# Optimization experiments

Measured on AMD Instinct MI355X. Metric: run time of the kernel, lower is better.

## Reference

```python
import jax, jax.numpy as jnp
import numpy as np

K_CLASSES = 5   # num support classes (5-way)
N_SHOT = 5      # supports per class


def setup_inputs() -> dict:
    key = jax.random.key(0)
    k0, k1, k2, k3 = jax.random.split(key, 4)
    b, bs, c, h, w = 32, K_CLASSES * N_SHOT, 512, 14, 14
    dk, dv = 128, 128
    return {
        "support_features": jax.random.normal(k0, (bs, c, h, w), jnp.float32),
        "query_features": jax.random.normal(k1, (b, c, h, w), jnp.float32),
        "support_labels": jnp.repeat(jnp.arange(K_CLASSES), N_SHOT).astype(jnp.int32),
        "W_qk": jax.random.normal(k2, (dk, c), jnp.float32) * 0.02,  # 1x1 conv weight
        "W_v": jax.random.normal(k3, (dv, c), jnp.float32) * 0.02,   # 1x1 conv weight
    }


def reference(support_features, query_features, support_labels, W_qk, W_v):
    scale = 1.0  # 1/temperature, temperature=1.0
    # 1x1 convs == channel-mixing einsums
    query_q = jnp.einsum('bchw,dc->bdhw', query_features, W_qk)
    query_v = jnp.einsum('bchw,dc->bdhw', query_features, W_v)
    supp_k = jnp.einsum('nchw,dc->ndhw', support_features, W_qk)
    supp_v = jnpveinsum = jnp.einsum('nchw,dc->ndhw', support_features, W_v)
    supp_v = jnpveinsum
    b, cv, h, w = query_v.shape

    # similarity over all supports: [b,h,w,n,i,j] (contracts dim_key)
    sim = jnp.einsum('bchw,ncij->bhwnij', query_q, supp_k) * scale

    # per-class masked softmax over the (n,i,j) axes restricted to that class's
    # supports == index_select + softmax in the original loop (labels balanced).
    cls_mask = support_labels[None, :] == jnp.arange(K_CLASSES)[:, None]  # [K,n]
    neg = jnp.finfo(sim.dtype).min
    sim_k = jnp.where(cls_mask[:, None, None, None, :, None, None], sim[None], neg)  # [K,b,h,w,n,i,j]
    attn = jax.nn.softmax(sim_k.reshape(K_CLASSES, b, h, w, -1), axis=-1)
    attn = attn.reshape(sim_k.shape)  # masked-out entries -> exactly 0

    # weighted sum of support values: [K,b,c,h,w]
    out = jnp.einsum('kbhwnij,ncij->kbchw', attn, supp_v)
    prototypes = jnp.transpose(out, (1, 0, 2, 3, 4)).reshape(b, K_CLASSES, -1)  # b k (c h w)
    query_v_flat = query_v.reshape(b, 1, -1)  # b () (c h w)
    return prototypes, query_v_flat
```

## Files before the change

### kernel.cpp

```cpp
#include <hip/hip_runtime.h>
#include <cstdint>
#include <cstddef>

#define NB   32
#define NSUP 25
#define KCLS 5
#define NC   512
#define ND   128
#define NP   196
#define JS   208
#define SHIFT 8.0f

#define KPITCH 272
#define KTILE  (16 * KPITCH)
#define KBUF   (2 * KTILE)
#define VPITCH 80
#define VBUF   (128 * VPITCH)
#define BUFSZ  (KBUF + VBUF)

#define NGRP   (NB * KCLS * 13)
#define PACC_F ((size_t)NGRP * 2 * 2048)
#define PSUM_F ((size_t)NGRP * 2 * 16)

typedef __attribute__((ext_vector_type(8))) short short8;
typedef __attribute__((ext_vector_type(4))) float floatx4;

__device__ inline short f2bf(float x) {
  union { float f; uint32_t u; } v; v.f = x;
  uint32_t r = (v.u + 0x7FFFu + ((v.u >> 16) & 1u)) >> 16;
  return (short)(r & 0xFFFFu);
}
__device__ inline uint32_t pk2(float a, float b) {
  return (uint32_t)(uint16_t)f2bf(a) | ((uint32_t)(uint16_t)f2bf(b) << 16);
}

__global__ __launch_bounds__(256) void wconv_kernel(
    const float* __restrict__ Wqk, const float* __restrict__ Wv,
    uint16_t* __restrict__ Whi)
{
  const int f = (blockIdx.x * 256 + (int)threadIdx.x) * 8;
  const float* src = (f < ND * NC) ? (Wqk + f) : (Wv + f - ND * NC);
  short8 hv;
  #pragma unroll
  for (int i = 0; i < 8; ++i) hv[i] = f2bf(src[i]);
  *(short8*)(Whi + f) = hv;
}

__global__ __launch_bounds__(256) void gemm_kernel(
    const float* __restrict__ supp, const float* __restrict__ qry,
    const uint16_t* __restrict__ Whi,
    uint16_t* __restrict__ Qt, uint16_t* __restrict__ Kt,
    uint16_t* __restrict__ Vt, float* __restrict__ outVq)
{
  __shared__ uint16_t xs[16 * 520];
  const int bx = blockIdx.x;
  const int t16 = bx % 13, img = bx / 13;
  const int tid = (int)threadIdx.x;
  const int w = tid >> 6, lane = tid & 63, ln = lane & 15, q = lane >> 4;
  const int d0 = w * 32;
  const int p0 = t16 * 16;

  const float* __restrict__ X = (img < NB)
      ? (qry  + (size_t)img * NC * NP)
      : (supp + (size_t)(img - NB) * NC * NP);

  #pragma unroll
  for (int k = 0; k < 4; ++k) {
    const int id = k * 256 + tid;
    const int cp = id >> 2;
    const int pq = id & 3;
    int pg = p0 + pq * 4; if (pg > NP - 4) pg = NP - 4;
    const floatx4 fa = *(const floatx4*)(X + (2 * cp) * NP + pg);
    const floatx4 fb = *(const floatx4*)(X + (2 * cp + 1) * NP + pg);
    #pragma unroll
    for (int i = 0; i < 4; ++i)
      *((uint32_t*)xs + (pq * 4 + i) * 260 + cp) = pk2(fa[i], fb[i]);
  }
  __syncthreads();

  floatx4 aQ[2], aV[2];
  #pragma unroll
  for (int nt = 0; nt < 2; ++nt) {
    aQ[nt] = (floatx4){0.f, 0.f, 0.f, 0.f};
    aV[nt] = (floatx4){0.f, 0.f, 0.f, 0.f};
  }

  for (int ks = 0; ks < 16; ++ks) {
    const short8 xh = *(const short8*)&xs[ln * 520 + ks * 32 + q * 8];
    #pragma unroll
    for (int nt = 0; nt < 2; ++nt) {
      const size_t wr = (size_t)(d0 + nt * 16 + ln) * NC + ks * 32 + q * 8;
      const short8 wqh = *(const short8*)(Whi + wr);
      aQ[nt] = __builtin_amdgcn_mfma_f32_16x16x32_bf16(xh, wqh, aQ[nt], 0, 0, 0);
      const short8 wvh = *(const short8*)(Whi + (size_t)ND * NC + wr);
      aV[nt] = __builtin_amdgcn_mfma_f32_16x16x32_bf16(wvh, xh, aV[nt], 0, 0, 0);
    }
  }

  if (img < NB) {
    #pragma unroll
    for (int nt = 0; nt < 2; ++nt)
      #pragma unroll
      for (int rr = 0; rr < 4; ++rr) {
        const int p = p0 + q * 4 + rr;
        if (p < NP)
          Qt[((size_t)img * NP + p) * ND + d0 + nt * 16 + ln] = (uint16_t)f2bf(aQ[nt][rr]);
      }
  } else {
    const int n = img - NB;
    #pragma unroll
    for (int nt = 0; nt < 2; ++nt)
      #pragma unroll
      for (int rr = 0; rr < 4; ++rr) {
        const int p = p0 + q * 4 + rr;
        Kt[((size_t)n * JS + p) * ND + d0 + nt * 16 + ln] = (uint16_t)f2bf(aQ[nt][rr]);
      }
  }
  const int p = p0 + ln;
  if (img < NB) {
    if (p < NP) {
      #pragma unroll
      for (int nt = 0; nt < 2; ++nt)
        #pragma unroll
        for (int rr = 0; rr < 4; ++rr)
          outVq[((size_t)img * ND + d0 + nt * 16 + q * 4 + rr) * NP + p] = aV[nt][rr];
    }
  } else {
    const int n = img - NB;
    #pragma unroll
    for (int nt = 0; nt < 2; ++nt)
      #pragma unroll
      for (int rr = 0; rr < 4; ++rr)
        Vt[((size_t)n * ND + d0 + nt * 16 + q * 4 + rr) * JS + p] = (uint16_t)f2bf(aV[nt][rr]);
  }
}

template <int NCHUNK, bool PART>
__global__ __launch_bounds__(256, 2) void attn_kernel(
    const uint16_t* __restrict__ Qt, const uint16_t* __restrict__ Kt,
    const uint16_t* __restrict__ Vt, const int* __restrict__ labels,
    float* __restrict__ out, float* __restrict__ pacc, float* __restrict__ psum)
{
  __shared__ __align__(16) char smem[2 * BUFSZ];

  const int bx = blockIdx.x;
  const int pt = bx % 13;
  const int rem = bx / 13;
  const int kc = rem % KCLS;
  const int rest = rem / KCLS;
  const int oct = PART ? (rest & 3) : rest;
  const int half = PART ? (rest >> 2) : 0;
  const int c0 = half * NCHUNK;
  const int b0 = oct * 8;
  const int p0 = pt * 16;
  const int tid = (int)threadIdx.x;
  const int w = tid >> 6, lane = tid & 63, ln = lane & 15, q = lane >> 4;
  const int bA = b0 + w * 2, bB = bA + 1;

  const int myl = (lane < NSUP) ? labels[lane] : -1;
  unsigned long long m = __ballot(myl == kc);
  int clsPack = 0;
  #pragma unroll
  for (int s = 0; s < 5; ++s) {
    const int n = (m != 0ull) ? (int)__builtin_ctzll(m) : 0;
    clsPack |= n << (6 * s);
    m &= (m - 1);
  }

  short8 aqA[4], aqB[4];
  {
    int p = p0 + ln; if (p > NP - 1) p = NP - 1;
    const uint16_t* baseA = Qt + ((size_t)bA * NP + p) * ND + q * 8;
    const uint16_t* baseB = Qt + ((size_t)bB * NP + p) * ND + q * 8;
    #pragma unroll
    for (int ks = 0; ks < 4; ++ks) {
      aqA[ks] = *(const short8*)(baseA + ks * 32);
      aqB[ks] = *(const short8*)(baseB + ks * 32);
    }
  }

  floatx4 accA[8], accB[8];
  #pragma unroll
  for (int dt = 0; dt < 8; ++dt) {
    accA[dt] = (floatx4){0.f, 0.f, 0.f, 0.f};
    accB[dt] = (floatx4){0.f, 0.f, 0.f, 0.f};
  }
  float SsA = 0.f, SsB = 0.f;

  const int alo = (ln + ((q & 1) << 5)) << 2;
  const bool hiTile = (q >= 2);

  int4 pf[4];
  {
    int nk[2], j0k[2], nv[2], jv[2];
    #pragma unroll
    for (int t = 0; t < 2; ++t) {
      const int tile16 = c0 * 2 + t;
      int s = tile16 / 13;
      j0k[t] = (tile16 - s * 13) * 16;
      if (s > 4) s = 4;
      nk[t] = (clsPack >> (6 * s)) & 63;
    }
    #pragma unroll
    for (int h = 0; h < 2; ++h) {
      const int ch = c0 * 32 + h * 16;
      int sv = ch / JS, jvv = ch - sv * JS;
      if (sv > 4) { sv = 4; jvv = 192; }
      nv[h] = (clsPack >> (6 * sv)) & 63;
      jv[h] = jvv;
    }
    #pragma unroll
    for (int pass = 0; pass < 4; ++pass) {
      const int slot = pass * 256 + tid;
      if (pass < 2) {
        const int t = slot >> 8, r = (slot >> 4) & 15, sc = slot & 15;
        pf[pass] = *(const int4*)(Kt + ((size_t)(nk[t] * JS + j0k[t] + r)) * ND + sc * 8);
      } else {
        const int vs = slot - 512;
        const int h = vs >> 8, d = (vs >> 1) & 127, sc2 = vs & 1;
        pf[pass] = *(const int4*)(Vt + ((size_t)(nv[h] * ND + d)) * JS + jv[h] + sc2 * 8);
      }
    }
    char* db = smem;
    #pragma unroll
    for (int pass = 0; pass < 4; ++pass) {
      const int slot = pass * 256 + tid;
      if (pass < 2) {
        const int t = slot >> 8, r = (slot >> 4) & 15, sc = slot & 15;
        *(int4*)(db + t * KTILE + r * KPITCH + sc * 16) = pf[pass];
      } else {
        const int vs = slot - 512;
        const int h = vs >> 8, d = (vs >> 1) & 127, sc2 = vs & 1;
        *(int4*)(db + KBUF + d * VPITCH + (h * 2 + sc2) * 16) = pf[pass];
      }
    }
  }
  __syncthreads();

  for (int li = 0; li < NCHUNK; ++li) {
    const int cc = c0 + li;
    const int nc = cc + 1;
    int nk[2], j0k[2], nv[2], jv[2];
    if (li < NCHUNK - 1) {
      #pragma unroll
      for (int t = 0; t < 2; ++t) {
        const int tile16 = nc * 2 + t;
        int s = tile16 / 13;
        j0k[t] = (tile16 - s * 13) * 16;
        if (s > 4) s = 4;
        nk[t] = (clsPack >> (6 * s)) & 63;
      }
      #pragma unroll
      for (int h = 0; h < 2; ++h) {
        const int ch = nc * 32 + h * 16;
        int sv = ch / JS, jvv = ch - sv * JS;
        if (sv > 4) { sv = 4; jvv = 192; }
        nv[h] = (clsPack >> (6 * sv)) & 63;
        jv[h] = jvv;
      }
      #pragma unroll
      for (int pass = 0; pass < 4; ++pass) {
        const int slot = pass * 256 + tid;
        if (pass < 2) {
          const int t = slot >> 8, r = (slot >> 4) & 15, sc = slot & 15;
          pf[pass] = *(const int4*)(Kt + ((size_t)(nk[t] * JS + j0k[t] + r)) * ND + sc * 8);
        } else {
          const int vs = slot - 512;
          const int h = vs >> 8, d = (vs >> 1) & 127, sc2 = vs & 1;
          pf[pass] = *(const int4*)(Vt + ((size_t)(nv[h] * ND + d)) * JS + jv[h] + sc2 * 8);
        }
      }
    }

    const char* kb = smem + (li & 1) * BUFSZ;
    const char* vb = kb + KBUF;

    short8 av[8];
    #pragma unroll
    for (int dt = 0; dt < 8; ++dt)
      av[dt] = *(const short8*)(vb + (dt * 16 + ln) * VPITCH + q * 16);

    short8 bk[2][4];
    #pragma unroll
    for (int t = 0; t < 2; ++t)
      #pragma unroll
      for (int ks = 0; ks < 4; ++ks)
        bk[t][ks] = *(const short8*)(kb + t * KTILE + ln * KPITCH + ks * 64 + q * 16);

    floatx4 e0A, e1A, e0B, e1B;
    #pragma unroll
    for (int t = 0; t < 2; ++t) {
      const int tile16 = cc * 2 + t;
      const int s = tile16 / 13;
      const int j0 = (tile16 - s * 13) * 16;
      const bool tval = (s < 5);
      floatx4 d4A = {0.f, 0.f, 0.f, 0.f};
      floatx4 d4B = {0.f, 0.f, 0.f, 0.f};
      #pragma unroll
      for (int ks = 0; ks < 4; ++ks) {
        d4A = __builtin_amdgcn_mfma_f32_16x16x32_bf16(bk[t][ks], aqA[ks], d4A, 0, 0, 0);
        d4B = __builtin_amdgcn_mfma_f32_16x16x32_bf16(bk[t][ks], aqB[ks], d4B, 0, 0, 0);
      }
      floatx4 evA, evB;
      #pragma unroll
      for (int r = 0; r < 4; ++r) {
        const int j = j0 + q * 4 + r;
        const bool val = (tval && j < NP);
        const float eA = val ? __expf(d4A[r] - SHIFT) : 0.f;
        const float eB = val ? __expf(d4B[r] - SHIFT) : 0.f;
        evA[r] = eA; SsA += eA;
        evB[r] = eB; SsB += eB;
      }
      if (t == 0) { e0A = evA; e0B = evB; } else { e1A = evA; e1B = evB; }
    }

    short8 bpA, bpB;
    #pragma unroll
    for (int r = 0; r < 4; ++r) {
      const uint32_t peA = pk2(e0A[r], e1A[r]);
      const int loA = __builtin_amdgcn_ds_bpermute(alo, (int)peA);
      const int hiA = __builtin_amdgcn_ds_bpermute(alo + 64, (int)peA);
      bpA[r]     = (short)(uint16_t)(hiTile ? (loA >> 16) : (loA & 0xFFFF));
      bpA[4 + r] = (short)(uint16_t)(hiTile ? (hiA >> 16) : (hiA & 0xFFFF));
      const uint32_t peB = pk2(e0B[r], e1B[r]);
      const int loB = __builtin_amdgcn_ds_bpermute(alo, (int)peB);
      const int hiB = __builtin_amdgcn_ds_bpermute(alo + 64, (int)peB);
      bpB[r]     = (short)(uint16_t)(hiTile ? (loB >> 16) : (loB & 0xFFFF));
      bpB[4 + r] = (short)(uint16_t)(hiTile ? (hiB >> 16) : (hiB & 0xFFFF));
    }

    #pragma unroll
    for (int dt = 0; dt < 8; ++dt) {
      accA[dt] = __builtin_amdgcn_mfma_f32_16x16x32_bf16(av[dt], bpA, accA[dt], 0, 0, 0);
      accB[dt] = __builtin_amdgcn_mfma_f32_16x16x32_bf16(av[dt], bpB, accB[dt], 0, 0, 0);
    }

    if (li < NCHUNK - 1) {
      char* db = smem + ((li + 1) & 1) * BUFSZ;
      #pragma unroll
      for (int pass = 0; pass < 4; ++pass) {
        const int slot = pass * 256 + tid;
        if (pass < 2) {
          const int t = slot >> 8, r = (slot >> 4) & 15, sc = slot & 15;
          *(int4*)(db + t * KTILE + r * KPITCH + sc * 16) = pf[pass];
        } else {
          const int vs = slot - 512;
          const int h = vs >> 8, d = (vs >> 1) & 127, sc2 = vs & 1;
          *(int4*)(db + KBUF + d * VPITCH + (h * 2 + sc2) * 16) = pf[pass];
        }
      }
    }
    __syncthreads();
  }

  float svA = SsA;
  svA += __shfl_xor(svA, 16);
  svA += __shfl_xor(svA, 32);
  float svB = SsB;
  svB += __shfl_xor(svB, 16);
  svB += __shfl_xor(svB, 32);

  if (PART) {
    const size_t grpA = (((size_t)(bA * KCLS + kc)) * 13 + pt) * 2 + half;
    const size_t grpB = (((size_t)(bB * KCLS + kc)) * 13 + pt) * 2 + half;
    float* paA = pacc + grpA * 2048;
    float* paB = pacc + grpB * 2048;
    #pragma unroll
    for (int dt = 0; dt < 8; ++dt)
      #pragma unroll
      for (int rr = 0; rr < 4; ++rr) {
        paA[(dt * 16 + q * 4 + rr) * 16 + ln] = accA[dt][rr];
        paB[(dt * 16 + q * 4 + rr) * 16 + ln] = accB[dt][rr];
      }
    if (q == 0) {
      psum[grpA * 16 + ln] = svA;
      psum[grpB * 16 + ln] = svB;
    }
  } else {
    const int pp = p0 + ln;
    if (pp < NP) {
      const float invA = 1.f / svA, invB = 1.f / svB;
      float* obA = out + ((size_t)(bA * KCLS + kc) * ND + q * 4) * NP + pp;
      float* obB = out + ((size_t)(bB * KCLS + kc) * ND + q * 4) * NP + pp;
      #pragma unroll
      for (int dt = 0; dt < 8; ++dt)
        #pragma unroll
        for (int rr = 0; rr < 4; ++rr) {
          obA[(size_t)(dt * 16 + rr) * NP] = accA[dt][rr] * invA;
          obB[(size_t)(dt * 16 + rr) * NP] = accB[dt][rr] * invB;
        }
    }
  }
}

__global__ __launch_bounds__(256) void merge_kernel(
    const float* __restrict__ pacc, const float* __restrict__ psum,
    float* __restrict__ out)
{
  const int bx = blockIdx.x;
  const int pt = bx % 13;
  const int rem = bx / 13;
  const int tid = (int)threadIdx.x;
  const int ln = tid & 15, dr = tid >> 4;
  const size_t g0 = (((size_t)rem) * 13 + pt) * 2;

  const float s = psum[g0 * 16 + ln] + psum[(g0 + 1) * 16 + ln];
  const int pp = pt * 16 + ln;
  if (pp >= NP) return;
  const float inv = 1.f / s;

  const float* pa0 = pacc + g0 * 2048;
  const float* pa1 = pacc + (g0 + 1) * 2048;
  float* ob = out + (size_t)rem * ND * NP + pp;
  #pragma unroll
  for (int i = 0; i < 8; ++i) {
    const int d = dr * 8 + i;
    ob[(size_t)d * NP] = (pa0[d * 16 + ln] + pa1[d * 16 + ln]) * inv;
  }
}

extern "C" void kernel_launch(void* const* d_in, const int* in_sizes, int n_in,
                              void* d_out, int out_size, void* d_ws, size_t ws_size,
                              hipStream_t stream) {
  const float* supp   = (const float*)d_in[0];
  const float* qry    = (const float*)d_in[1];
  const int*   labels = (const int*)d_in[2];
  const float* Wqk    = (const float*)d_in[3];
  const float* Wv     = (const float*)d_in[4];
  float* out = (float*)d_out;

  uint16_t* Whi = (uint16_t*)d_ws;
  uint16_t* Qt  = Whi + (size_t)2 * ND * NC;
  uint16_t* Kt  = Qt  + (size_t)NB * NP * ND;
  uint16_t* Vt  = Kt  + (size_t)NSUP * JS * ND;
  float* pacc   = (float*)(Vt + (size_t)NSUP * ND * JS);
  float* psum   = pacc + PACC_F;
  const size_t need = (size_t)((char*)(psum + PSUM_F) - (char*)d_ws);
  float* outVq = out + (size_t)NB * KCLS * ND * NP;

  wconv_kernel<<<64, 256, 0, stream>>>(Wqk, Wv, Whi);
  gemm_kernel<<<741, 256, 0, stream>>>(supp, qry, Whi, Qt, Kt, Vt, outVq);
  if (ws_size >= need) {
    attn_kernel<17, true><<<520, 256, 0, stream>>>(Qt, Kt, Vt, labels, out, pacc, psum);
    merge_kernel<<<2080, 256, 0, stream>>>(pacc, psum, out);
  } else {
    attn_kernel<34, false><<<260, 256, 0, stream>>>(Qt, Kt, Vt, labels, out, nullptr, nullptr);
  }
}
```

Before: 164.9 us.

## Stage K/V tiles via direct global-to-LDS loads with XOR-swizzled layout

Replaces the register-staged prefetch of K and V tiles (global load into registers, then a later LDS store) with global_load_lds direct copies into a swizzled, unpadded double buffer. This removes the register pressure and the extra LDS-store pass. Tile index decoding now uses incremental counters instead of divisions. It also swaps software bf16 rounding for the hardware v_cvt_pk_bf16_f32 instruction and adds s_setprio around the MFMA blocks. The risks are in correctness: the swizzle must match the fragment reads, and the V tile addressing at the segment tail changes from clamping to using raw offsets.

After: 169.5 us. 2.8% more time.

```diff
diff --git a/kernel.cpp b/kernel.cpp
--- a/kernel.cpp
+++ b/kernel.cpp
@@ -11,12 +11,8 @@
 #define JS   208
 #define SHIFT 8.0f
 
-#define KPITCH 272
-#define KTILE  (16 * KPITCH)
-#define KBUF   (2 * KTILE)
-#define VPITCH 80
-#define VBUF   (128 * VPITCH)
-#define BUFSZ  (KBUF + VBUF)
+#define ABUF   16384
+#define VOFF   8192
 
 #define NGRP   (NB * KCLS * 13)
 #define PACC_F ((size_t)NGRP * 2 * 2048)
@@ -30,8 +26,15 @@
   uint32_t r = (v.u + 0x7FFFu + ((v.u >> 16) & 1u)) >> 16;
   return (short)(r & 0xFFFFu);
 }
-__device__ inline uint32_t pk2(float a, float b) {
-  return (uint32_t)(uint16_t)f2bf(a) | ((uint32_t)(uint16_t)f2bf(b) << 16);
+__device__ inline uint32_t cvtpk(float lo, float hi) {
+  uint32_t r;
+  asm("v_cvt_pk_bf16_f32 %0, %1, %2" : "=v"(r) : "v"(lo), "v"(hi));
+  return r;
+}
+__device__ __forceinline__ void gl_lds16(const uint16_t* g, char* l) {
+  __builtin_amdgcn_global_load_lds(
+      (const __attribute__((address_space(1))) uint32_t*)g,
+      (__attribute__((address_space(3))) uint32_t*)l, 16, 0, 0);
 }
 
 __global__ __launch_bounds__(256) void wconv_kernel(
@@ -74,7 +77,7 @@
     const floatx4 fb = *(const floatx4*)(X + (2 * cp + 1) * NP + pg);
     #pragma unroll
     for (int i = 0; i < 4; ++i)
-      *((uint32_t*)xs + (pq * 4 + i) * 260 + cp) = pk2(fa[i], fb[i]);
+      *((uint32_t*)xs + (pq * 4 + i) * 260 + cp) = cvtpk(fa[i], fb[i]);
   }
   __syncthreads();
 
@@ -135,13 +138,42 @@
   }
 }
 
+
+#define DECODE2() do {                                                         \
+    _Pragma("unroll")                                                          \
+    for (int t_ = 0; t_ < 2; ++t_) {                                           \
+      dS[t_] = s_ctr; dJ[t_] = j_ctr;                                          \
+      const int sc_ = s_ctr > 4 ? 4 : s_ctr;                                   \
+      dN[t_] = (clsPack >> (6 * sc_)) & 63;                                    \
+      j_ctr += 16; if (j_ctr >= JS) { j_ctr -= JS; s_ctr += 1; }               \
+    }                                                                          \
+  } while (0)
+
+#define STAGE(DB) do {                                                         \
+    if (w < 2) {                                                               \
+      const int kb_ = (dN[w] * JS + dJ[w]) * ND;                               \
+      _Pragma("unroll")                                                        \
+      for (int i_ = 0; i_ < 4; ++i_)                                           \
+        gl_lds16(Kt + kb_ + dKoff[i_], (DB) + w * 4096 + i_ * 1024);           \
+    } else {                                                                   \
+      const int vA_ = dN[0] * (ND * JS) + dJ[0];                               \
+      const int vB_ = dN[1] * (ND * JS) + dJ[1];                               \
+      const int vs_ = hb ? vB_ : vA_;                                          \
+      const int i2b_ = (w & 1) * 4;                                            \
+      _Pragma("unroll")                                                        \
+      for (int k_ = 0; k_ < 4; ++k_)                                           \
+        gl_lds16(Vt + vs_ + (i2b_ + k_) * (16 * JS) + vrow,                    \
+                 (DB) + VOFF + (i2b_ + k_) * 1024);                            \
+    }                                                                          \
+  } while (0)
+
 template <int NCHUNK, bool PART>
 __global__ __launch_bounds__(256, 2) void attn_kernel(
     const uint16_t* __restrict__ Qt, const uint16_t* __restrict__ Kt,
     const uint16_t* __restrict__ Vt, const int* __restrict__ labels,
     float* __restrict__ out, float* __restrict__ pacc, float* __restrict__ psum)
 {
-  __shared__ __align__(16) char smem[2 * BUFSZ];
+  __shared__ __align__(16) char smem[2 * ABUF];
 
   const int bx = blockIdx.x;
   const int pt = bx % 13;
@@ -166,6 +198,7 @@
     clsPack |= n << (6 * s);
     m &= (m - 1);
   }
+  clsPack = __builtin_amdgcn_readfirstlane(clsPack);
 
   short8 aqA[4], aqB[4];
   {
@@ -190,122 +223,71 @@
   const int alo = (ln + ((q & 1) << 5)) << 2;
   const bool hiTile = (q >= 2);
 
-  int4 pf[4];
-  {
-    int nk[2], j0k[2], nv[2], jv[2];
+  const int rK = lane >> 4, scK = lane & 15;
+  int dKoff[4];
+  #pragma unroll
+  for (int i = 0; i < 4; ++i) {
+    const int r = 4 * i + rK;
+    dKoff[i] = r * ND + ((scK ^ (r & 7)) * 8);
+  }
+  const int dV = lane >> 2, s2 = lane & 3;
+  const int s2p = s2 ^ ((dV >> 1) & 3);
+  const int hb = s2p >> 1;
+  const int vrow = dV * JS + (s2p & 1) * 8;
+
+  int kfr[4];
+  #pragma unroll
+  for (int ks = 0; ks < 4; ++ks)
+    kfr[ks] = ln * 256 + (((ks * 4 + q) ^ (ln & 7)) << 4);
+  const int avb = VOFF + ln * 64 + ((q ^ ((ln >> 1) & 3)) << 4);
+
+  int s_ctr = (c0 * 2) / 13;
+  int j_ctr = (c0 * 2 - s_ctr * 13) * 16;
+  int dS[2], dJ[2], dN[2], cS[2], cJ[2];
+
+  DECODE2();
+  STAGE(smem);
+  __syncthreads();
+
+  for (int it = 0; it < NCHUNK; ++it) {
+    #pragma unroll
+    for (int i = 0; i < 2; ++i) { cS[i] = dS[i]; cJ[i] = dJ[i]; }
+    if (it < NCHUNK - 1) {
+      DECODE2();
+      STAGE(smem + ((it + 1) & 1) * ABUF);
+    }
+
+    const char* cb = smem + (it & 1) * ABUF;
+
+    short8 av[8];
+    #pragma unroll
+    for (int dt = 0; dt < 8; ++dt)
+      av[dt] = *(const short8*)(cb + avb + dt * 1024);
+
+    short8 bk[2][4];
+    #pragma unroll
+    for (int t = 0; t < 2; ++t)
+      #pragma unroll
+      for (int ks = 0; ks < 4; ++ks)
+        bk[t][ks] = *(const short8*)(cb + kfr[ks] + t * 4096);
+
+    floatx4 e0A, e1A, e0B, e1B;
     #pragma unroll
     for (int t = 0; t < 2; ++t) {
-      const int tile16 = c0 * 2 + t;
-      int s = tile16 / 13;
-      j0k[t] = (tile16 - s * 13) * 16;
-      if (s > 4) s = 4;
-      nk[t] = (clsPack >> (6 * s)) & 63;
-    }
-    #pragma unroll
-    for (int h = 0; h < 2; ++h) {
-      const int ch = c0 * 32 + h * 16;
-      int sv = ch / JS, jvv = ch - sv * JS;
-      if (sv > 4) { sv = 4; jvv = 192; }
-      nv[h] = (clsPack >> (6 * sv)) & 63;
-      jv[h] = jvv;
-    }
-    #pragma unroll
-    for (int pass = 0; pass < 4; ++pass) {
-      const int slot = pass * 256 + tid;
-      if (pass < 2) {
-        const int t = slot >> 8, r = (slot >> 4) & 15, sc = slot & 15;
-        pf[pass] = *(const int4*)(Kt + ((size_t)(nk[t] * JS + j0k[t] + r)) * ND + sc * 8);
-      } else {
-        const int vs = slot - 512;
-        const int h = vs >> 8, d = (vs >> 1) & 127, sc2 = vs & 1;
-        pf[pass] = *(const int4*)(Vt + ((size_t)(nv[h] * ND + d)) * JS + jv[h] + sc2 * 8);
-      }
-    }
-    char* db = smem;
-    #pragma unroll
-    for (int pass = 0; pass < 4; ++pass) {
-      const int slot = pass * 256 + tid;
-      if (pass < 2) {
-        const int t = slot >> 8, r = (slot >> 4) & 15, sc = slot & 15;
-        *(int4*)(db + t * KTILE + r * KPITCH + sc * 16) = pf[pass];
-      } else {
-        const int vs = slot - 512;
-        const int h = vs >> 8, d = (vs >> 1) & 127, sc2 = vs & 1;
-        *(int4*)(db + KBUF + d * VPITCH + (h * 2 + sc2) * 16) = pf[pass];
-      }
-    }
-  }
-  __syncthreads();
-
-  for (int li = 0; li < NCHUNK; ++li) {
-    const int cc = c0 + li;
-    const int nc = cc + 1;
-    int nk[2], j0k[2], nv[2], jv[2];
-    if (li < NCHUNK - 1) {
-      #pragma unroll
-      for (int t = 0; t < 2; ++t) {
-        const int tile16 = nc * 2 + t;
-        int s = tile16 / 13;
-        j0k[t] = (tile16 - s * 13) * 16;
-        if (s > 4) s = 4;
-        nk[t] = (clsPack >> (6 * s)) & 63;
-      }
-      #pragma unroll
-      for (int h = 0; h < 2; ++h) {
-        const int ch = nc * 32 + h * 16;
-        int sv = ch / JS, jvv = ch - sv * JS;
-        if (sv > 4) { sv = 4; jvv = 192; }
-        nv[h] = (clsPack >> (6 * sv)) & 63;
-        jv[h] = jvv;
-      }
-      #pragma unroll
-      for (int pass = 0; pass < 4; ++pass) {
-        const int slot = pass * 256 + tid;
-        if (pass < 2) {
-          const int t = slot >> 8, r = (slot >> 4) & 15, sc = slot & 15;
-          pf[pass] = *(const int4*)(Kt + ((size_t)(nk[t] * JS + j0k[t] + r)) * ND + sc * 8);
-        } else {
-          const int vs = slot - 512;
-          const int h = vs >> 8, d = (vs >> 1) & 127, sc2 = vs & 1;
-          pf[pass] = *(const int4*)(Vt + ((size_t)(nv[h] * ND + d)) * JS + jv[h] + sc2 * 8);
-        }
-      }
-    }
-
-    const char* kb = smem + (li & 1) * BUFSZ;
-    const char* vb = kb + KBUF;
-
-    short8 av[8];
-    #pragma unroll
-    for (int dt = 0; dt < 8; ++dt)
-      av[dt] = *(const short8*)(vb + (dt * 16 + ln) * VPITCH + q * 16);
-
-    short8 bk[2][4];
-    #pragma unroll
-    for (int t = 0; t < 2; ++t)
-      #pragma unroll
-      for (int ks = 0; ks < 4; ++ks)
-        bk[t][ks] = *(const short8*)(kb + t * KTILE + ln * KPITCH + ks * 64 + q * 16);
-
-    floatx4 e0A, e1A, e0B, e1B;
-    #pragma unroll
-    for (int t = 0; t < 2; ++t) {
-      const int tile16 = cc * 2 + t;
-      const int s = tile16 / 13;
-      const int j0 = (tile16 - s * 13) * 16;
-      const bool tval = (s < 5);
       floatx4 d4A = {0.f, 0.f, 0.f, 0.f};
       floatx4 d4B = {0.f, 0.f, 0.f, 0.f};
+      __builtin_amdgcn_s_setprio(1);
       #pragma unroll
       for (int ks = 0; ks < 4; ++ks) {
         d4A = __builtin_amdgcn_mfma_f32_16x16x32_bf16(bk[t][ks], aqA[ks], d4A, 0, 0, 0);
         d4B = __builtin_amdgcn_mfma_f32_16x16x32_bf16(bk[t][ks], aqB[ks], d4B, 0, 0, 0);
       }
+      __builtin_amdgcn_s_setprio(0);
       floatx4 evA, evB;
       #pragma unroll
       for (int r = 0; r < 4; ++r) {
-        const int j = j0 + q * 4 + r;
-        const bool val = (tval && j < NP);
+        const int j = cJ[t] + q * 4 + r;
+        const bool val = (cS[t] < 5 && j < NP);
         const float eA = val ? __expf(d4A[r] - SHIFT) : 0.f;
         const float eB = val ? __expf(d4B[r] - SHIFT) : 0.f;
         evA[r] = eA; SsA += eA;
@@ -317,39 +299,26 @@
     short8 bpA, bpB;
     #pragma unroll
     for (int r = 0; r < 4; ++r) {
-      const uint32_t peA = pk2(e0A[r], e1A[r]);
+      const uint32_t peA = cvtpk(e0A[r], e1A[r]);
       const int loA = __builtin_amdgcn_ds_bpermute(alo, (int)peA);
       const int hiA = __builtin_amdgcn_ds_bpermute(alo + 64, (int)peA);
       bpA[r]     = (short)(uint16_t)(hiTile ? (loA >> 16) : (loA & 0xFFFF));
       bpA[4 + r] = (short)(uint16_t)(hiTile ? (hiA >> 16) : (hiA & 0xFFFF));
-      const uint32_t peB = pk2(e0B[r], e1B[r]);
+      const uint32_t peB = cvtpk(e0B[r], e1B[r]);
       const int loB = __builtin_amdgcn_ds_bpermute(alo, (int)peB);
       const int hiB = __builtin_amdgcn_ds_bpermute(alo + 64, (int)peB);
       bpB[r]     = (short)(uint16_t)(hiTile ? (loB >> 16) : (loB & 0xFFFF));
       bpB[4 + r] = (short)(uint16_t)(hiTile ? (hiB >> 16) : (hiB & 0xFFFF));
     }
 
+    __builtin_amdgcn_s_setprio(1);
     #pragma unroll
     for (int dt = 0; dt < 8; ++dt) {
       accA[dt] = __builtin_amdgcn_mfma_f32_16x16x32_bf16(av[dt], bpA, accA[dt], 0, 0, 0);
       accB[dt] = __builtin_amdgcn_mfma_f32_16x16x32_bf16(av[dt], bpB, accB[dt], 0, 0, 0);
     }
-
-    if (li < NCHUNK - 1) {
-      char* db = smem + ((li + 1) & 1) * BUFSZ;
-      #pragma unroll
-      for (int pass = 0; pass < 4; ++pass) {
-        const int slot = pass * 256 + tid;
-        if (pass < 2) {
-          const int t = slot >> 8, r = (slot >> 4) & 15, sc = slot & 15;
-          *(int4*)(db + t * KTILE + r * KPITCH + sc * 16) = pf[pass];
-        } else {
-          const int vs = slot - 512;
-          const int h = vs >> 8, d = (vs >> 1) & 127, sc2 = vs & 1;
-          *(int4*)(db + KBUF + d * VPITCH + (h * 2 + sc2) * 16) = pf[pass];
-        }
-      }
-    }
+    __builtin_amdgcn_s_setprio(0);
+
     __syncthreads();
   }
 
```

## Load V fragments directly from global into registers and use hardware bf16 pack

Applied to the files above, without the earlier changes.

Stops staging the V tile through shared memory. Each lane now loads its MFMA A-operand fragments for V straight from global memory at the start of each chunk, and the shared buffer holds only the double-buffered K tiles. This removes the LDS writes and reads for V and shrinks LDS use, which can help occupancy. In exchange, V loads are issued in the same iteration they are used, so they are no longer prefetched a chunk ahead and their latency may be exposed. The software float-to-bf16 rounding is also replaced with the v_cvt_pk_bf16_f32 instruction.

Measured after the change: 175.2 us. 1.06x slower.

```diff
diff --git a/kernel.cpp b/kernel.cpp
--- a/kernel.cpp
+++ b/kernel.cpp
@@ -14,9 +14,6 @@
 #define KPITCH 272
 #define KTILE  (16 * KPITCH)
 #define KBUF   (2 * KTILE)
-#define VPITCH 80
-#define VBUF   (128 * VPITCH)
-#define BUFSZ  (KBUF + VBUF)
 
 #define NGRP   (NB * KCLS * 13)
 #define PACC_F ((size_t)NGRP * 2 * 2048)
@@ -30,8 +27,10 @@
   uint32_t r = (v.u + 0x7FFFu + ((v.u >> 16) & 1u)) >> 16;
   return (short)(r & 0xFFFFu);
 }
-__device__ inline uint32_t pk2(float a, float b) {
-  return (uint32_t)(uint16_t)f2bf(a) | ((uint32_t)(uint16_t)f2bf(b) << 16);
+__device__ inline uint32_t cvtpk(float lo, float hi) {
+  uint32_t r;
+  asm("v_cvt_pk_bf16_f32 %0, %1, %2" : "=v"(r) : "v"(lo), "v"(hi));
+  return r;
 }
 
 __global__ __launch_bounds__(256) void wconv_kernel(
@@ -74,7 +73,7 @@
     const floatx4 fb = *(const floatx4*)(X + (2 * cp + 1) * NP + pg);
     #pragma unroll
     for (int i = 0; i < 4; ++i)
-      *((uint32_t*)xs + (pq * 4 + i) * 260 + cp) = pk2(fa[i], fb[i]);
+      *((uint32_t*)xs + (pq * 4 + i) * 260 + cp) = cvtpk(fa[i], fb[i]);
   }
   __syncthreads();
 
@@ -141,7 +140,7 @@
     const uint16_t* __restrict__ Vt, const int* __restrict__ labels,
     float* __restrict__ out, float* __restrict__ pacc, float* __restrict__ psum)
 {
-  __shared__ __align__(16) char smem[2 * BUFSZ];
+  __shared__ __align__(16) char smem[2 * KBUF];
 
   const int bx = blockIdx.x;
   const int pt = bx % 13;
@@ -190,9 +189,10 @@
   const int alo = (ln + ((q & 1) << 5)) << 2;
   const bool hiTile = (q >= 2);
 
-  int4 pf[4];
+  int4 pf[2];
+  int cnv[2], cjv[2];
   {
-    int nk[2], j0k[2], nv[2], jv[2];
+    int nk[2], j0k[2];
     #pragma unroll
     for (int t = 0; t < 2; ++t) {
       const int tile16 = c0 * 2 + t;
@@ -206,33 +206,20 @@
       const int ch = c0 * 32 + h * 16;
       int sv = ch / JS, jvv = ch - sv * JS;
       if (sv > 4) { sv = 4; jvv = 192; }
-      nv[h] = (clsPack >> (6 * sv)) & 63;
-      jv[h] = jvv;
-    }
-    #pragma unroll
-    for (int pass = 0; pass < 4; ++pass) {
+      cnv[h] = (clsPack >> (6 * sv)) & 63;
+      cjv[h] = jvv;
+    }
+    #pragma unroll
+    for (int pass = 0; pass < 2; ++pass) {
       const int slot = pass * 256 + tid;
-      if (pass < 2) {
-        const int t = slot >> 8, r = (slot >> 4) & 15, sc = slot & 15;
-        pf[pass] = *(const int4*)(Kt + ((size_t)(nk[t] * JS + j0k[t] + r)) * ND + sc * 8);
-      } else {
-        const int vs = slot - 512;
-        const int h = vs >> 8, d = (vs >> 1) & 127, sc2 = vs & 1;
-        pf[pass] = *(const int4*)(Vt + ((size_t)(nv[h] * ND + d)) * JS + jv[h] + sc2 * 8);
-      }
-    }
-    char* db = smem;
-    #pragma unroll
-    for (int pass = 0; pass < 4; ++pass) {
+      const int t = slot >> 8, r = (slot >> 4) & 15, sc = slot & 15;
+      pf[pass] = *(const int4*)(Kt + ((size_t)(nk[t] * JS + j0k[t] + r)) * ND + sc * 8);
+    }
+    #pragma unroll
+    for (int pass = 0; pass < 2; ++pass) {
       const int slot = pass * 256 + tid;
-      if (pass < 2) {
-        const int t = slot >> 8, r = (slot >> 4) & 15, sc = slot & 15;
-        *(int4*)(db + t * KTILE + r * KPITCH + sc * 16) = pf[pass];
-      } else {
-        const int vs = slot - 512;
-        const int h = vs >> 8, d = (vs >> 1) & 127, sc2 = vs & 1;
-        *(int4*)(db + KBUF + d * VPITCH + (h * 2 + sc2) * 16) = pf[pass];
-      }
+      const int t = slot >> 8, r = (slot >> 4) & 15, sc = slot & 15;
+      *(int4*)(smem + t * KTILE + r * KPITCH + sc * 16) = pf[pass];
     }
   }
   __syncthreads();
@@ -240,8 +227,19 @@
   for (int li = 0; li < NCHUNK; ++li) {
     const int cc = c0 + li;
     const int nc = cc + 1;
-    int nk[2], j0k[2], nv[2], jv[2];
+
+    const int nvh = hiTile ? cnv[1] : cnv[0];
+    const int jvh = hiTile ? cjv[1] : cjv[0];
+    const uint16_t* vr = Vt + ((size_t)nvh * ND + ln) * JS + jvh + (q & 1) * 8;
+    short8 av[8];
+    #pragma unroll
+    for (int dt = 0; dt < 8; ++dt)
+      av[dt] = *(const short8*)(vr + (size_t)(dt * 16) * JS);
+    __builtin_amdgcn_sched_barrier(0);
+
+    int nnv[2], njv[2];
     if (li < NCHUNK - 1) {
+      int nk[2], j0k[2];
       #pragma unroll
       for (int t = 0; t < 2; ++t) {
         const int tile16 = nc * 2 + t;
@@ -255,30 +253,18 @@
         const int ch = nc * 32 + h * 16;
         int sv = ch / JS, jvv = ch - sv * JS;
         if (sv > 4) { sv = 4; jvv = 192; }
-        nv[h] = (clsPack >> (6 * sv)) & 63;
-        jv[h] = jvv;
-      }
-      #pragma unroll
-      for (int pass = 0; pass < 4; ++pass) {
+        nnv[h] = (clsPack >> (6 * sv)) & 63;
+        njv[h] = jvv;
+      }
+      #pragma unroll
+      for (int pass = 0; pass < 2; ++pass) {
         const int slot = pass * 256 + tid;
-        if (pass < 2) {
-          const int t = slot >> 8, r = (slot >> 4) & 15, sc = slot & 15;
-          pf[pass] = *(const int4*)(Kt + ((size_t)(nk[t] * JS + j0k[t] + r)) * ND + sc * 8);
-        } else {
-          const int vs = slot - 512;
-          const int h = vs >> 8, d = (vs >> 1) & 127, sc2 = vs & 1;
-          pf[pass] = *(const int4*)(Vt + ((size_t)(nv[h] * ND + d)) * JS + jv[h] + sc2 * 8);
-        }
-      }
-    }
-
-    const char* kb = smem + (li & 1) * BUFSZ;
-    const char* vb = kb + KBUF;
-
-    short8 av[8];
-    #pragma unroll
-    for (int dt = 0; dt < 8; ++dt)
-      av[dt] = *(const short8*)(vb + (dt * 16 + ln) * VPITCH + q * 16);
+        const int t = slot >> 8, r = (slot >> 4) & 15, sc = slot & 15;
+        pf[pass] = *(const int4*)(Kt + ((size_t)(nk[t] * JS + j0k[t] + r)) * ND + sc * 8);
+      }
+    }
+
+    const char* kb = smem + (li & 1) * KBUF;
 
     short8 bk[2][4];
     #pragma unroll
@@ -317,12 +303,12 @@
     short8 bpA, bpB;
     #pragma unroll
     for (int r = 0; r < 4; ++r) {
-      const uint32_t peA = pk2(e0A[r], e1A[r]);
+      const uint32_t peA = cvtpk(e0A[r], e1A[r]);
       const int loA = __builtin_amdgcn_ds_bpermute(alo, (int)peA);
       const int hiA = __builtin_amdgcn_ds_bpermute(alo + 64, (int)peA);
       bpA[r]     = (short)(uint16_t)(hiTile ? (loA >> 16) : (loA & 0xFFFF));
       bpA[4 + r] = (short)(uint16_t)(hiTile ? (hiA >> 16) : (hiA & 0xFFFF));
-      const uint32_t peB = pk2(e0B[r], e1B[r]);
+      const uint32_t peB = cvtpk(e0B[r], e1B[r]);
       const int loB = __builtin_amdgcn_ds_bpermute(alo, (int)peB);
       const int hiB = __builtin_amdgcn_ds_bpermute(alo + 64, (int)peB);
       bpB[r]     = (short)(uint16_t)(hiTile ? (loB >> 16) : (loB & 0xFFFF));
@@ -336,19 +322,15 @@
     }
 
     if (li < NCHUNK - 1) {
-      char* db = smem + ((li + 1) & 1) * BUFSZ;
-      #pragma unroll
-      for (int pass = 0; pass < 4; ++pass) {
+      char* db = smem + ((li + 1) & 1) * KBUF;
+      #pragma unroll
+      for (int pass = 0; pass < 2; ++pass) {
         const int slot = pass * 256 + tid;
-        if (pass < 2) {
-          const int t = slot >> 8, r = (slot >> 4) & 15, sc = slot & 15;
-          *(int4*)(db + t * KTILE + r * KPITCH + sc * 16) = pf[pass];
-        } else {
-          const int vs = slot - 512;
-          const int h = vs >> 8, d = (vs >> 1) & 127, sc2 = vs & 1;
-          *(int4*)(db + KBUF + d * VPITCH + (h * 2 + sc2) * 16) = pf[pass];
-        }
-      }
+        const int t = slot >> 8, r = (slot >> 4) & 15, sc = slot & 15;
+        *(int4*)(db + t * KTILE + r * KPITCH + sc * 16) = pf[pass];
+      }
+      cnv[0] = nnv[0]; cnv[1] = nnv[1];
+      cjv[0] = njv[0]; cjv[1] = njv[1];
     }
     __syncthreads();
   }
```

## Fuse split-K merge into attention via atomic last-block finalize; use hw bf16 pack

Applied to the files above, without the earlier changes.

Removes the separate merge kernel. Each attention block still writes its partial accumulators and sums, then bumps a per-tile atomic counter. The block that arrives second reads its partner's partial, combines it with its own register accumulators, normalizes, and writes the output directly. This saves one launch and half of the partial-buffer reads. It relies on the flag counters starting even and on the atomic-parity protocol staying correct across repeated calls. It also replaces the software bf16 round-and-pack with the v_cvt_pk_bf16_f32 instruction.

Measured after the change: 254.5 us. 1.54x slower.

```diff
diff --git a/kernel.cpp b/kernel.cpp
--- a/kernel.cpp
+++ b/kernel.cpp
@@ -21,6 +21,7 @@
 #define NGRP   (NB * KCLS * 13)
 #define PACC_F ((size_t)NGRP * 2 * 2048)
 #define PSUM_F ((size_t)NGRP * 2 * 16)
+#define NPAIR  (4 * KCLS * 13)
 
 typedef __attribute__((ext_vector_type(8))) short short8;
 typedef __attribute__((ext_vector_type(4))) float floatx4;
@@ -30,8 +31,10 @@
   uint32_t r = (v.u + 0x7FFFu + ((v.u >> 16) & 1u)) >> 16;
   return (short)(r & 0xFFFFu);
 }
-__device__ inline uint32_t pk2(float a, float b) {
-  return (uint32_t)(uint16_t)f2bf(a) | ((uint32_t)(uint16_t)f2bf(b) << 16);
+__device__ inline uint32_t cvtpk(float lo, float hi) {
+  uint32_t r;
+  asm("v_cvt_pk_bf16_f32 %0, %1, %2" : "=v"(r) : "v"(lo), "v"(hi));
+  return r;
 }
 
 __global__ __launch_bounds__(256) void wconv_kernel(
@@ -74,7 +77,7 @@
     const floatx4 fb = *(const floatx4*)(X + (2 * cp + 1) * NP + pg);
     #pragma unroll
     for (int i = 0; i < 4; ++i)
-      *((uint32_t*)xs + (pq * 4 + i) * 260 + cp) = pk2(fa[i], fb[i]);
+      *((uint32_t*)xs + (pq * 4 + i) * 260 + cp) = cvtpk(fa[i], fb[i]);
   }
   __syncthreads();
 
@@ -139,7 +142,8 @@
 __global__ __launch_bounds__(256, 2) void attn_kernel(
     const uint16_t* __restrict__ Qt, const uint16_t* __restrict__ Kt,
     const uint16_t* __restrict__ Vt, const int* __restrict__ labels,
-    float* __restrict__ out, float* __restrict__ pacc, float* __restrict__ psum)
+    float* __restrict__ out, float* __restrict__ pacc, float* __restrict__ psum,
+    int* __restrict__ flags)
 {
   __shared__ __align__(16) char smem[2 * BUFSZ];
 
@@ -317,12 +321,12 @@
     short8 bpA, bpB;
     #pragma unroll
     for (int r = 0; r < 4; ++r) {
-      const uint32_t peA = pk2(e0A[r], e1A[r]);
+      const uint32_t peA = cvtpk(e0A[r], e1A[r]);
       const int loA = __builtin_amdgcn_ds_bpermute(alo, (int)peA);
       const int hiA = __builtin_amdgcn_ds_bpermute(alo + 64, (int)peA);
       bpA[r]     = (short)(uint16_t)(hiTile ? (loA >> 16) : (loA & 0xFFFF));
       bpA[4 + r] = (short)(uint16_t)(hiTile ? (hiA >> 16) : (hiA & 0xFFFF));
-      const uint32_t peB = pk2(e0B[r], e1B[r]);
+      const uint32_t peB = cvtpk(e0B[r], e1B[r]);
       const int loB = __builtin_amdgcn_ds_bpermute(alo, (int)peB);
       const int hiB = __builtin_amdgcn_ds_bpermute(alo + 64, (int)peB);
       bpB[r]     = (short)(uint16_t)(hiTile ? (loB >> 16) : (loB & 0xFFFF));
@@ -361,10 +365,10 @@
   svB += __shfl_xor(svB, 32);
 
   if (PART) {
-    const size_t grpA = (((size_t)(bA * KCLS + kc)) * 13 + pt) * 2 + half;
-    const size_t grpB = (((size_t)(bB * KCLS + kc)) * 13 + pt) * 2 + half;
-    float* paA = pacc + grpA * 2048;
-    float* paB = pacc + grpB * 2048;
+    const size_t gA = (((size_t)(bA * KCLS + kc)) * 13 + pt) * 2 + half;
+    const size_t gB = (((size_t)(bB * KCLS + kc)) * 13 + pt) * 2 + half;
+    float* paA = pacc + gA * 2048;
+    float* paB = pacc + gB * 2048;
     #pragma unroll
     for (int dt = 0; dt < 8; ++dt)
       #pragma unroll
@@ -373,8 +377,38 @@
         paB[(dt * 16 + q * 4 + rr) * 16 + ln] = accB[dt][rr];
       }
     if (q == 0) {
-      psum[grpA * 16 + ln] = svA;
-      psum[grpB * 16 + ln] = svB;
+      psum[gA * 16 + ln] = svA;
+      psum[gB * 16 + ln] = svB;
+    }
+    __threadfence();
+    __syncthreads();
+    if (tid == 0)
+      ((int*)smem)[0] = atomicAdd(&flags[(oct * KCLS + kc) * 13 + pt], 1);
+    __syncthreads();
+    const int old = ((int*)smem)[0];
+    if (old & 1) {
+      __threadfence();
+      const size_t gAo = (((size_t)(bA * KCLS + kc)) * 13 + pt) * 2 + (1 - half);
+      const size_t gBo = (((size_t)(bB * KCLS + kc)) * 13 + pt) * 2 + (1 - half);
+      const float svAt = svA + psum[gAo * 16 + ln];
+      const float svBt = svB + psum[gBo * 16 + ln];
+      const int pp = p0 + ln;
+      if (pp < NP) {
+        const float invA = 1.f / svAt, invB = 1.f / svBt;
+        const float* qaA = pacc + gAo * 2048;
+        const float* qaB = pacc + gBo * 2048;
+        float* obA = out + ((size_t)(bA * KCLS + kc) * ND + q * 4) * NP + pp;
+        float* obB = out + ((size_t)(bB * KCLS + kc) * ND + q * 4) * NP + pp;
+        #pragma unroll
+        for (int dt = 0; dt < 8; ++dt)
+          #pragma unroll
+          for (int rr = 0; rr < 4; ++rr) {
+            obA[(size_t)(dt * 16 + rr) * NP] =
+                (accA[dt][rr] + qaA[(dt * 16 + q * 4 + rr) * 16 + ln]) * invA;
+            obB[(size_t)(dt * 16 + rr) * NP] =
+                (accB[dt][rr] + qaB[(dt * 16 + q * 4 + rr) * 16 + ln]) * invB;
+          }
+      }
     }
   } else {
     const int pp = p0 + ln;
@@ -390,32 +424,6 @@
           obB[(size_t)(dt * 16 + rr) * NP] = accB[dt][rr] * invB;
         }
     }
-  }
-}
-
-__global__ __launch_bounds__(256) void merge_kernel(
-    const float* __restrict__ pacc, const float* __restrict__ psum,
-    float* __restrict__ out)
-{
-  const int bx = blockIdx.x;
-  const int pt = bx % 13;
-  const int rem = bx / 13;
-  const int tid = (int)threadIdx.x;
-  const int ln = tid & 15, dr = tid >> 4;
-  const size_t g0 = (((size_t)rem) * 13 + pt) * 2;
-
-  const float s = psum[g0 * 16 + ln] + psum[(g0 + 1) * 16 + ln];
-  const int pp = pt * 16 + ln;
-  if (pp >= NP) return;
-  const float inv = 1.f / s;
-
-  const float* pa0 = pacc + g0 * 2048;
-  const float* pa1 = pacc + (g0 + 1) * 2048;
-  float* ob = out + (size_t)rem * ND * NP + pp;
-  #pragma unroll
-  for (int i = 0; i < 8; ++i) {
-    const int d = dr * 8 + i;
-    ob[(size_t)d * NP] = (pa0[d * 16 + ln] + pa1[d * 16 + ln]) * inv;
   }
 }
 
@@ -435,15 +443,15 @@
   uint16_t* Vt  = Kt  + (size_t)NSUP * JS * ND;
   float* pacc   = (float*)(Vt + (size_t)NSUP * ND * JS);
   float* psum   = pacc + PACC_F;
-  const size_t need = (size_t)((char*)(psum + PSUM_F) - (char*)d_ws);
+  int*   flags  = (int*)(psum + PSUM_F);
+  const size_t need = (size_t)((char*)(flags + NPAIR) - (char*)d_ws);
   float* outVq = out + (size_t)NB * KCLS * ND * NP;
 
   wconv_kernel<<<64, 256, 0, stream>>>(Wqk, Wv, Whi);
   gemm_kernel<<<741, 256, 0, stream>>>(supp, qry, Whi, Qt, Kt, Vt, outVq);
   if (ws_size >= need) {
-    attn_kernel<17, true><<<520, 256, 0, stream>>>(Qt, Kt, Vt, labels, out, pacc, psum);
-    merge_kernel<<<2080, 256, 0, stream>>>(pacc, psum, out);
+    attn_kernel<17, true><<<520, 256, 0, stream>>>(Qt, Kt, Vt, labels, out, pacc, psum, flags);
   } else {
-    attn_kernel<34, false><<<260, 256, 0, stream>>>(Qt, Kt, Vt, labels, out, nullptr, nullptr);
-  }
-}
+    attn_kernel<34, false><<<260, 256, 0, stream>>>(Qt, Kt, Vt, labels, out, nullptr, nullptr, nullptr);
+  }
+}
```
